# Optimization experiments

Measured on AMD Instinct MI355X. Metric: run time of the kernel, lower is better.

Reference implementation:

```python
import jax, jax.numpy as jnp
import numpy as np

N, T, U, D, V = 8, 200, 100, 512, 500


def setup_inputs() -> dict:
    key = jax.random.key(0)
    k1, k2, k3, k4 = jax.random.split(key, 4)
    encoder_out = jax.random.normal(k1, (N, T, D), dtype=jnp.float32)
    decoder_out = jax.random.normal(k2, (N, U, D), dtype=jnp.float32)
    # nn.Linear(input_dim, output_dim): weight (V, D), bias (V,)
    bound = 1.0 / np.sqrt(D)
    W = jax.random.uniform(k3, (V, D), minval=-bound, maxval=bound, dtype=jnp.float32)
    b = jax.random.uniform(k4, (V,), minval=-bound, maxval=bound, dtype=jnp.float32)
    return {"encoder_out": encoder_out, "decoder_out": decoder_out, "W": W, "b": b}


def reference(encoder_out, decoder_out, W, b):
    # broadcast add: (N,T,1,D) + (N,1,U,D) -> (N,T,U,D)
    x = encoder_out[:, :, None, :] + decoder_out[:, None, :, :]
    activations = jnp.tanh(x)
    # linear: (N,T,U,D) @ (D,V) + b -> (N,T,U,V)
    logits = jnp.einsum("ntud,vd->ntuv", activations, W) + b
    return logits
```

## Files before the change

### kernel.cpp

```cpp
#include <hip/hip_runtime.h>
#include <hip/hip_bf16.h>


#define NB 8
#define TT 200
#define UU 100
#define DD 512
#define VV 500
#define VP 512
#define BM 64
#define BK 32
#define KSTEPS 16
#define THREADS 256
#define LDA 40
#define MROWS (NB*TT*UU)
#define MBLOCKS (MROWS/BM)

typedef __attribute__((ext_vector_type(4))) float  f32x4;
typedef __attribute__((ext_vector_type(8))) short  s16x8;

__device__ __forceinline__ unsigned short f2bf(float f) {
    unsigned int u = __builtin_bit_cast(unsigned int, f);
    u = (u + 0x7FFFu + ((u >> 16) & 1u)) >> 16;
    return (unsigned short)u;
}

__device__ __forceinline__ float fast_tanh(float x) {
    float e = __expf(2.0f * x);
    return 1.0f - 2.0f * __builtin_amdgcn_rcpf(e + 1.0f);
}

__global__ void prep_w(const float* __restrict__ W, unsigned short* __restrict__ Wt) {
    int idx = blockIdx.x * 256 + threadIdx.x;
    int k = idx & 511;
    int v = idx >> 9;
    float val = (v < VV) ? W[v * DD + k] : 0.0f;
    Wt[(k >> 5) * (VP * BK) + v * BK + (k & 31)] = f2bf(val);
}

__global__ __launch_bounds__(THREADS, 2) void joiner_kernel(
    const float* __restrict__ enc, const float* __restrict__ dec,
    const unsigned short* __restrict__ Wt, const float* __restrict__ bias,
    float* __restrict__ out)
{
    __shared__ __align__(16) char smem[32000];
    unsigned short* lA0 = (unsigned short*)smem;
    unsigned short* lA1 = (unsigned short*)(smem + BM * LDA * 2);

    const int tid  = threadIdx.x;
    const int mb   = blockIdx.x;
    const int lane = tid & 63;
    const int wn   = tid >> 6;
    const int lr   = lane & 15;
    const int lk   = lane >> 4;

    const int srow = tid >> 2;
    const int sk   = (tid & 3) << 3;

    int r   = mb * BM + srow;
    int n   = r / (TT * UU);
    int rem = r - n * (TT * UU);
    int t   = rem / UU;
    int u   = rem - t * UU;
    const float* ep = enc + (n * TT + t) * DD + sk;
    const float* dp = dec + (n * UU + u) * DD + sk;

    f32x4 e0, e1, d0, d1;

    e0 = *(const f32x4*)(ep);     e1 = *(const f32x4*)(ep + 4);
    d0 = *(const f32x4*)(dp);     d1 = *(const f32x4*)(dp + 4);
    {
        s16x8 av;
        #pragma unroll
        for (int j = 0; j < 4; ++j) av[j]     = (short)f2bf(fast_tanh(e0[j] + d0[j]));
        #pragma unroll
        for (int j = 0; j < 4; ++j) av[4 + j] = (short)f2bf(fast_tanh(e1[j] + d1[j]));
        *(s16x8*)(&lA0[srow * LDA + sk]) = av;
    }
    e0 = *(const f32x4*)(ep + BK);     e1 = *(const f32x4*)(ep + BK + 4);
    d0 = *(const f32x4*)(dp + BK);     d1 = *(const f32x4*)(dp + BK + 4);
    __syncthreads();

    f32x4 acc[4][8];
    #pragma unroll
    for (int m = 0; m < 4; ++m)
        #pragma unroll
        for (int f = 0; f < 8; ++f)
            acc[m][f] = (f32x4){0.f, 0.f, 0.f, 0.f};

    const unsigned short* wptr = Wt + (wn * 128 + lr) * BK + lk * 8;

    for (int kc = 0; kc < KSTEPS; ++kc) {
        unsigned short* lCur = (kc & 1) ? lA1 : lA0;
        unsigned short* lNxt = (kc & 1) ? lA0 : lA1;

        s16x8 bF[8];
        #pragma unroll
        for (int f = 0; f < 8; ++f)
            bF[f] = *(const s16x8*)(wptr + kc * (VP * BK) + f * (16 * BK));

        s16x8 aF[4];
        #pragma unroll
        for (int m = 0; m < 4; ++m)
            aF[m] = *(const s16x8*)(&lCur[(m * 16 + lr) * LDA + lk * 8]);

        if (kc < KSTEPS - 1) {
            s16x8 av;
            #pragma unroll
            for (int j = 0; j < 4; ++j) av[j]     = (short)f2bf(fast_tanh(e0[j] + d0[j]));
            #pragma unroll
            for (int j = 0; j < 4; ++j) av[4 + j] = (short)f2bf(fast_tanh(e1[j] + d1[j]));
            *(s16x8*)(&lNxt[srow * LDA + sk]) = av;
            if (kc < KSTEPS - 2) {
                const float* ep2 = ep + (kc + 2) * BK;
                const float* dp2 = dp + (kc + 2) * BK;
                e0 = *(const f32x4*)(ep2);     e1 = *(const f32x4*)(ep2 + 4);
                d0 = *(const f32x4*)(dp2);     d1 = *(const f32x4*)(dp2 + 4);
            }
        }

        __builtin_amdgcn_s_setprio(1);
        #pragma unroll
        for (int m = 0; m < 4; ++m)
            #pragma unroll
            for (int f = 0; f < 8; ++f)
                acc[m][f] = __builtin_amdgcn_mfma_f32_16x16x32_bf16(aF[m], bF[f], acc[m][f], 0, 0, 0);
        __builtin_amdgcn_s_setprio(0);

        __syncthreads();
    }

    float bv[8];
    #pragma unroll
    for (int f = 0; f < 8; ++f) {
        int v = wn * 128 + f * 16 + lr;
        bv[f] = (v < VV) ? bias[v] : 0.0f;
    }

    float* lchunk = (float*)smem;
    float* outbase = out + (long)mb * BM * VV;

    for (int m = 0; m < 4; ++m) {
        __syncthreads();
        #pragma unroll
        for (int f = 0; f < 8; ++f) {
            int v = wn * 128 + f * 16 + lr;
            if (v < VV) {
                #pragma unroll
                for (int q = 0; q < 4; ++q)
                    lchunk[(lk * 4 + q) * VV + v] = acc[m][f][q] + bv[f];
            }
        }
        __syncthreads();
        float* dst = outbase + m * 16 * VV;
        #pragma unroll
        for (int i = 0; i < 8; ++i) {
            int c = i * THREADS + tid;
            if (c < 2000)
                *(f32x4*)(dst + c * 4) = *(const f32x4*)(lchunk + c * 4);
        }
    }
}

extern "C" void kernel_launch(void* const* d_in, const int* in_sizes, int n_in,
                              void* d_out, int out_size, void* d_ws, size_t ws_size,
                              hipStream_t stream) {
    const float* enc = (const float*)d_in[0];
    const float* dec = (const float*)d_in[1];
    const float* W   = (const float*)d_in[2];
    const float* b   = (const float*)d_in[3];
    float* out = (float*)d_out;
    unsigned short* Wt = (unsigned short*)d_ws;

    prep_w<<<dim3((VP * DD) / 256), dim3(256), 0, stream>>>(W, Wt);
    joiner_kernel<<<dim3(MBLOCKS), dim3(THREADS), 0, stream>>>(enc, dec, Wt, b, out);
}
```

Baseline: 144.6 us.

## Split vocab dimension across two blocks to halve accumulators and raise occupancy

Each block now covers 256 of the 500 vocab columns, using a 2D grid, instead of all of them. This halves the per-wave accumulator and B-fragment registers, and the launch bounds are raised to allow 3 blocks per SM. The staging buffer for the output is resized to a padded 264-float row. The cost is that every block recomputes the tanh activations for its rows and loads encoder and decoder data twice, so activation work and input traffic double.

```diff
diff --git a/kernel.cpp b/kernel.cpp
--- a/kernel.cpp
+++ b/kernel.cpp
@@ -9,10 +9,12 @@
 #define VV 500
 #define VP 512
 #define BM 64
+#define BNB 256
 #define BK 32
 #define KSTEPS 16
 #define THREADS 256
 #define LDA 40
+#define LCH 264
 #define MROWS (NB*TT*UU)
 #define MBLOCKS (MROWS/BM)
 
@@ -38,17 +40,18 @@
     Wt[(k >> 5) * (VP * BK) + v * BK + (k & 31)] = f2bf(val);
 }
 
-__global__ __launch_bounds__(THREADS, 2) void joiner_kernel(
+__global__ __launch_bounds__(THREADS, 3) void joiner_kernel(
     const float* __restrict__ enc, const float* __restrict__ dec,
     const unsigned short* __restrict__ Wt, const float* __restrict__ bias,
     float* __restrict__ out)
 {
-    __shared__ __align__(16) char smem[32000];
+    __shared__ __align__(16) char smem[16 * LCH * 4];
     unsigned short* lA0 = (unsigned short*)smem;
     unsigned short* lA1 = (unsigned short*)(smem + BM * LDA * 2);
 
     const int tid  = threadIdx.x;
     const int mb   = blockIdx.x;
+    const int vb   = blockIdx.y;
     const int lane = tid & 63;
     const int wn   = tid >> 6;
     const int lr   = lane & 15;
@@ -81,22 +84,22 @@
     d0 = *(const f32x4*)(dp + BK);     d1 = *(const f32x4*)(dp + BK + 4);
     __syncthreads();
 
-    f32x4 acc[4][8];
+    f32x4 acc[4][4];
     #pragma unroll
     for (int m = 0; m < 4; ++m)
         #pragma unroll
-        for (int f = 0; f < 8; ++f)
+        for (int f = 0; f < 4; ++f)
             acc[m][f] = (f32x4){0.f, 0.f, 0.f, 0.f};
 
-    const unsigned short* wptr = Wt + (wn * 128 + lr) * BK + lk * 8;
+    const unsigned short* wptr = Wt + (vb * BNB + wn * 64 + lr) * BK + lk * 8;
 
     for (int kc = 0; kc < KSTEPS; ++kc) {
         unsigned short* lCur = (kc & 1) ? lA1 : lA0;
         unsigned short* lNxt = (kc & 1) ? lA0 : lA1;
 
-        s16x8 bF[8];
+        s16x8 bF[4];
         #pragma unroll
-        for (int f = 0; f < 8; ++f)
+        for (int f = 0; f < 4; ++f)
             bF[f] = *(const s16x8*)(wptr + kc * (VP * BK) + f * (16 * BK));
 
         s16x8 aF[4];
@@ -123,41 +126,44 @@
         #pragma unroll
         for (int m = 0; m < 4; ++m)
             #pragma unroll
-            for (int f = 0; f < 8; ++f)
+            for (int f = 0; f < 4; ++f)
                 acc[m][f] = __builtin_amdgcn_mfma_f32_16x16x32_bf16(aF[m], bF[f], acc[m][f], 0, 0, 0);
         __builtin_amdgcn_s_setprio(0);
 
         __syncthreads();
     }
 
-    float bv[8];
+    float bv[4];
     #pragma unroll
-    for (int f = 0; f < 8; ++f) {
-        int v = wn * 128 + f * 16 + lr;
+    for (int f = 0; f < 4; ++f) {
+        int v = vb * BNB + wn * 64 + f * 16 + lr;
         bv[f] = (v < VV) ? bias[v] : 0.0f;
     }
 
     float* lchunk = (float*)smem;
-    float* outbase = out + (long)mb * BM * VV;
+    const int slabcols = (vb == 0) ? BNB : (VV - BNB);
+    const int segmax   = slabcols >> 2;
+    float* outbase = out + (long)mb * BM * VV + vb * BNB;
 
-    for (int m = 0; m < 4; ++m) {
+    for (int c = 0; c < 4; ++c) {
         __syncthreads();
         #pragma unroll
-        for (int f = 0; f < 8; ++f) {
-            int v = wn * 128 + f * 16 + lr;
-            if (v < VV) {
-                #pragma unroll
-                for (int q = 0; q < 4; ++q)
-                    lchunk[(lk * 4 + q) * VV + v] = acc[m][f][q] + bv[f];
-            }
+        for (int f = 0; f < 4; ++f) {
+            int vloc = wn * 64 + f * 16 + lr;
+            #pragma unroll
+            for (int q = 0; q < 4; ++q)
+                lchunk[(lk * 4 + q) * LCH + vloc] = acc[c][f][q] + bv[f];
         }
         __syncthreads();
-        float* dst = outbase + m * 16 * VV;
+        float* dst = outbase + c * 16 * VV;
         #pragma unroll
-        for (int i = 0; i < 8; ++i) {
-            int c = i * THREADS + tid;
-            if (c < 2000)
-                *(f32x4*)(dst + c * 4) = *(const f32x4*)(lchunk + c * 4);
+        for (int i = 0; i < 4; ++i) {
+            int idx = i * THREADS + tid;
+            int row = idx >> 6;
+            int seg = idx & 63;
+            if (seg < segmax)
+                *(f32x4*)(dst + row * VV + seg * 4) =
+                    *(const f32x4*)(lchunk + row * LCH + seg * 4);
         }
     }
 }
@@ -173,5 +179,5 @@
     unsigned short* Wt = (unsigned short*)d_ws;
 
     prep_w<<<dim3((VP * DD) / 256), dim3(256), 0, stream>>>(W, Wt);
-    joiner_kernel<<<dim3(MBLOCKS), dim3(THREADS), 0, stream>>>(enc, dec, Wt, b, out);
+    joiner_kernel<<<dim3(MBLOCKS, 2), dim3(THREADS), 0, stream>>>(enc, dec, Wt, b, out);
 }
```

Result: slower. 157.3 us (+8.8%).

## Split tanh activation into separate pass and tile GEMM over vocab halves

Applied to the files above, without the earlier changes.

When the workspace is large enough, the code first materialises the bf16 tanh activations for all 160k rows to global memory. A separate GEMM kernel then reads A fragments directly from global memory and splits the vocab dimension across two blocks, using 128x256 tiles with 512 threads. This removes per-block redundant tanh work and LDS staging of A, but adds roughly 160 MB of extra global writes and reads. The old fused kernel stays as the fallback when the workspace is too small.

```diff
diff --git a/kernel.cpp b/kernel.cpp
--- a/kernel.cpp
+++ b/kernel.cpp
@@ -8,13 +8,7 @@
 #define DD 512
 #define VV 500
 #define VP 512
-#define BM 64
-#define BK 32
-#define KSTEPS 16
-#define THREADS 256
-#define LDA 40
 #define MROWS (NB*TT*UU)
-#define MBLOCKS (MROWS/BM)
 
 typedef __attribute__((ext_vector_type(4))) float  f32x4;
 typedef __attribute__((ext_vector_type(8))) short  s16x8;
@@ -35,17 +29,133 @@
     int k = idx & 511;
     int v = idx >> 9;
     float val = (v < VV) ? W[v * DD + k] : 0.0f;
-    Wt[(k >> 5) * (VP * BK) + v * BK + (k & 31)] = f2bf(val);
-}
-
-__global__ __launch_bounds__(THREADS, 2) void joiner_kernel(
+    Wt[(k >> 5) * (VP * 32) + v * 32 + (k & 31)] = f2bf(val);
+}
+
+
+#define T1GRID 4096
+__global__ __launch_bounds__(256) void tanh_act(
+    const float* __restrict__ enc, const float* __restrict__ dec,
+    unsigned short* __restrict__ act)
+{
+    const int total = MROWS * (DD / 8);
+    for (int idx = blockIdx.x * 256 + threadIdx.x; idx < total;
+         idx += T1GRID * 256) {
+        int row = idx >> 6;
+        int k8  = (idx & 63) << 3;
+        int n   = row / (TT * UU);
+        int rem = row - n * (TT * UU);
+        int t   = rem / UU;
+        int u   = rem - t * UU;
+        const float* ep = enc + (n * TT + t) * DD + k8;
+        const float* dp = dec + (n * UU + u) * DD + k8;
+        f32x4 e0 = *(const f32x4*)(ep);
+        f32x4 e1 = *(const f32x4*)(ep + 4);
+        f32x4 d0 = *(const f32x4*)(dp);
+        f32x4 d1 = *(const f32x4*)(dp + 4);
+        s16x8 av;
+        #pragma unroll
+        for (int j = 0; j < 4; ++j) av[j]     = (short)f2bf(fast_tanh(e0[j] + d0[j]));
+        #pragma unroll
+        for (int j = 0; j < 4; ++j) av[4 + j] = (short)f2bf(fast_tanh(e1[j] + d1[j]));
+        *(s16x8*)(act + (long)row * DD + k8) = av;
+    }
+}
+
+#define GLCH 264
+__global__ __launch_bounds__(512, 4) void gemm_split(
+    const unsigned short* __restrict__ act, const unsigned short* __restrict__ Wt,
+    const float* __restrict__ bias, float* __restrict__ out)
+{
+    __shared__ __align__(16) float lchunk[32 * GLCH];
+
+    const int tid  = threadIdx.x;
+    const int mb   = blockIdx.x;
+    const int vb   = blockIdx.y;
+    const int lane = tid & 63;
+    const int w    = tid >> 6;
+    const int wm   = w >> 2;
+    const int wn   = w & 3;
+    const int lr   = lane & 15;
+    const int lk   = lane >> 4;
+
+    f32x4 acc[4][4];
+    #pragma unroll
+    for (int m = 0; m < 4; ++m)
+        #pragma unroll
+        for (int f = 0; f < 4; ++f)
+            acc[m][f] = (f32x4){0.f, 0.f, 0.f, 0.f};
+
+    const unsigned short* aptr = act + (long)(mb * 128 + wm * 64 + lr) * DD + lk * 8;
+    const unsigned short* wptr = Wt + (vb * 256 + wn * 64 + lr) * 32 + lk * 8;
+
+    for (int kc = 0; kc < 16; ++kc) {
+        s16x8 aF[4], bF[4];
+        #pragma unroll
+        for (int f = 0; f < 4; ++f)
+            bF[f] = *(const s16x8*)(wptr + kc * (VP * 32) + f * (16 * 32));
+        #pragma unroll
+        for (int m = 0; m < 4; ++m)
+            aF[m] = *(const s16x8*)(aptr + (long)(m * 16) * DD + kc * 32);
+
+        __builtin_amdgcn_s_setprio(1);
+        #pragma unroll
+        for (int m = 0; m < 4; ++m)
+            #pragma unroll
+            for (int f = 0; f < 4; ++f)
+                acc[m][f] = __builtin_amdgcn_mfma_f32_16x16x32_bf16(aF[m], bF[f], acc[m][f], 0, 0, 0);
+        __builtin_amdgcn_s_setprio(0);
+    }
+
+    float bv[4];
+    #pragma unroll
+    for (int f = 0; f < 4; ++f) {
+        int v = vb * 256 + wn * 64 + f * 16 + lr;
+        bv[f] = (v < VV) ? bias[v] : 0.0f;
+    }
+    const int slabcols = (vb == 0) ? 256 : (VV - 256);
+    const int segmax   = slabcols >> 2;
+    float* outbase = out + (long)mb * 128 * VV + vb * 256;
+
+    for (int c = 0; c < 4; ++c) {
+        if (c) __syncthreads();
+        if (wm == (c >> 1)) {
+            #pragma unroll
+            for (int mm = 0; mm < 2; ++mm) {
+                int m = (c & 1) * 2 + mm;
+                #pragma unroll
+                for (int f = 0; f < 4; ++f) {
+                    int vloc = wn * 64 + f * 16 + lr;
+                    #pragma unroll
+                    for (int q = 0; q < 4; ++q)
+                        lchunk[(mm * 16 + lk * 4 + q) * GLCH + vloc] = acc[m][f][q] + bv[f];
+                }
+            }
+        }
+        __syncthreads();
+        float* dst = outbase + (long)c * 32 * VV;
+        #pragma unroll
+        for (int i = 0; i < 4; ++i) {
+            int idx2 = i * 512 + tid;
+            int rw = idx2 >> 6;
+            int sg = idx2 & 63;
+            if (sg < segmax)
+                *(f32x4*)(dst + (long)rw * VV + sg * 4) =
+                    *(const f32x4*)(lchunk + rw * GLCH + sg * 4);
+        }
+    }
+}
+
+#define FBM 64
+#define FLDA 40
+__global__ __launch_bounds__(256, 2) void joiner_fused(
     const float* __restrict__ enc, const float* __restrict__ dec,
     const unsigned short* __restrict__ Wt, const float* __restrict__ bias,
     float* __restrict__ out)
 {
     __shared__ __align__(16) char smem[32000];
     unsigned short* lA0 = (unsigned short*)smem;
-    unsigned short* lA1 = (unsigned short*)(smem + BM * LDA * 2);
+    unsigned short* lA1 = (unsigned short*)(smem + FBM * FLDA * 2);
 
     const int tid  = threadIdx.x;
     const int mb   = blockIdx.x;
@@ -53,11 +163,10 @@
     const int wn   = tid >> 6;
     const int lr   = lane & 15;
     const int lk   = lane >> 4;
-
     const int srow = tid >> 2;
     const int sk   = (tid & 3) << 3;
 
-    int r   = mb * BM + srow;
+    int r   = mb * FBM + srow;
     int n   = r / (TT * UU);
     int rem = r - n * (TT * UU);
     int t   = rem / UU;
@@ -66,7 +175,6 @@
     const float* dp = dec + (n * UU + u) * DD + sk;
 
     f32x4 e0, e1, d0, d1;
-
     e0 = *(const f32x4*)(ep);     e1 = *(const f32x4*)(ep + 4);
     d0 = *(const f32x4*)(dp);     d1 = *(const f32x4*)(dp + 4);
     {
@@ -75,10 +183,10 @@
         for (int j = 0; j < 4; ++j) av[j]     = (short)f2bf(fast_tanh(e0[j] + d0[j]));
         #pragma unroll
         for (int j = 0; j < 4; ++j) av[4 + j] = (short)f2bf(fast_tanh(e1[j] + d1[j]));
-        *(s16x8*)(&lA0[srow * LDA + sk]) = av;
-    }
-    e0 = *(const f32x4*)(ep + BK);     e1 = *(const f32x4*)(ep + BK + 4);
-    d0 = *(const f32x4*)(dp + BK);     d1 = *(const f32x4*)(dp + BK + 4);
+        *(s16x8*)(&lA0[srow * FLDA + sk]) = av;
+    }
+    e0 = *(const f32x4*)(ep + 32);     e1 = *(const f32x4*)(ep + 36);
+    d0 = *(const f32x4*)(dp + 32);     d1 = *(const f32x4*)(dp + 36);
     __syncthreads();
 
     f32x4 acc[4][8];
@@ -88,32 +196,32 @@
         for (int f = 0; f < 8; ++f)
             acc[m][f] = (f32x4){0.f, 0.f, 0.f, 0.f};
 
-    const unsigned short* wptr = Wt + (wn * 128 + lr) * BK + lk * 8;
-
-    for (int kc = 0; kc < KSTEPS; ++kc) {
+    const unsigned short* wptr = Wt + (wn * 128 + lr) * 32 + lk * 8;
+
+    for (int kc = 0; kc < 16; ++kc) {
         unsigned short* lCur = (kc & 1) ? lA1 : lA0;
         unsigned short* lNxt = (kc & 1) ? lA0 : lA1;
 
         s16x8 bF[8];
         #pragma unroll
         for (int f = 0; f < 8; ++f)
-            bF[f] = *(const s16x8*)(wptr + kc * (VP * BK) + f * (16 * BK));
+            bF[f] = *(const s16x8*)(wptr + kc * (VP * 32) + f * (16 * 32));
 
         s16x8 aF[4];
         #pragma unroll
         for (int m = 0; m < 4; ++m)
-            aF[m] = *(const s16x8*)(&lCur[(m * 16 + lr) * LDA + lk * 8]);
-
-        if (kc < KSTEPS - 1) {
+            aF[m] = *(const s16x8*)(&lCur[(m * 16 + lr) * FLDA + lk * 8]);
+
+        if (kc < 15) {
             s16x8 av;
             #pragma unroll
             for (int j = 0; j < 4; ++j) av[j]     = (short)f2bf(fast_tanh(e0[j] + d0[j]));
             #pragma unroll
             for (int j = 0; j < 4; ++j) av[4 + j] = (short)f2bf(fast_tanh(e1[j] + d1[j]));
-            *(s16x8*)(&lNxt[srow * LDA + sk]) = av;
-            if (kc < KSTEPS - 2) {
-                const float* ep2 = ep + (kc + 2) * BK;
-                const float* dp2 = dp + (kc + 2) * BK;
+            *(s16x8*)(&lNxt[srow * FLDA + sk]) = av;
+            if (kc < 14) {
+                const float* ep2 = ep + (kc + 2) * 32;
+                const float* dp2 = dp + (kc + 2) * 32;
                 e0 = *(const f32x4*)(ep2);     e1 = *(const f32x4*)(ep2 + 4);
                 d0 = *(const f32x4*)(dp2);     d1 = *(const f32x4*)(dp2 + 4);
             }
@@ -138,7 +246,7 @@
     }
 
     float* lchunk = (float*)smem;
-    float* outbase = out + (long)mb * BM * VV;
+    float* outbase = out + (long)mb * FBM * VV;
 
     for (int m = 0; m < 4; ++m) {
         __syncthreads();
@@ -155,7 +263,7 @@
         float* dst = outbase + m * 16 * VV;
         #pragma unroll
         for (int i = 0; i < 8; ++i) {
-            int c = i * THREADS + tid;
+            int c = i * 256 + tid;
             if (c < 2000)
                 *(f32x4*)(dst + c * 4) = *(const f32x4*)(lchunk + c * 4);
         }
@@ -170,8 +278,19 @@
     const float* W   = (const float*)d_in[2];
     const float* b   = (const float*)d_in[3];
     float* out = (float*)d_out;
-    unsigned short* Wt = (unsigned short*)d_ws;
-
-    prep_w<<<dim3((VP * DD) / 256), dim3(256), 0, stream>>>(W, Wt);
-    joiner_kernel<<<dim3(MBLOCKS), dim3(THREADS), 0, stream>>>(enc, dec, Wt, b, out);
-}
+
+    const size_t actBytes = (size_t)MROWS * DD * 2;
+    const size_t wtBytes  = (size_t)VP * DD * 2;
+
+    if (ws_size >= actBytes + wtBytes) {
+        unsigned short* act = (unsigned short*)d_ws;
+        unsigned short* Wt  = (unsigned short*)((char*)d_ws + actBytes);
+        prep_w<<<dim3((VP * DD) / 256), dim3(256), 0, stream>>>(W, Wt);
+        tanh_act<<<dim3(T1GRID), dim3(256), 0, stream>>>(enc, dec, act);
+        gemm_split<<<dim3(MROWS / 128, 2), dim3(512), 0, stream>>>(act, Wt, b, out);
+    } else {
+        unsigned short* Wt = (unsigned short*)d_ws;
+        prep_w<<<dim3((VP * DD) / 256), dim3(256), 0, stream>>>(W, Wt);
+        joiner_fused<<<dim3(MROWS / FBM), dim3(256), 0, stream>>>(enc, dec, Wt, b, out);
+    }
+}
```

Result: slower. 350.7 us (+142.6%).

## Compute tanh activations directly into MFMA A-fragments, drop LDS staging

Applied to the files above, without the earlier changes.

Each wave now loads encoder/decoder values for its own A-fragment rows, applies tanh and packs to bf16 with v_cvt_pk_bf16_f32 directly in registers. This removes the LDS double buffer and the per-k-step __syncthreads. The tanh is also rewritten with exp2 and an fma. In exchange, each of the 4 waves recomputes the same 64xK tanh tile, so transcendental work is four times higher. Global loads also lose the one-step-ahead prefetch and now sit on the critical path before the MFMAs.

```diff
diff --git a/kernel.cpp b/kernel.cpp
--- a/kernel.cpp
+++ b/kernel.cpp
@@ -12,12 +12,12 @@
 #define BK 32
 #define KSTEPS 16
 #define THREADS 256
-#define LDA 40
 #define MROWS (NB*TT*UU)
 #define MBLOCKS (MROWS/BM)
 
-typedef __attribute__((ext_vector_type(4))) float  f32x4;
-typedef __attribute__((ext_vector_type(8))) short  s16x8;
+typedef __attribute__((ext_vector_type(4))) float         f32x4;
+typedef __attribute__((ext_vector_type(8))) short         s16x8;
+typedef __attribute__((ext_vector_type(4))) unsigned int  u32x4;
 
 __device__ __forceinline__ unsigned short f2bf(float f) {
     unsigned int u = __builtin_bit_cast(unsigned int, f);
@@ -25,9 +25,15 @@
     return (unsigned short)u;
 }
 
+__device__ __forceinline__ unsigned int cvt_pk_bf16(float a, float b) {
+    unsigned int r;
+    asm("v_cvt_pk_bf16_f32 %0, %1, %2" : "=v"(r) : "v"(a), "v"(b));
+    return r;
+}
+
 __device__ __forceinline__ float fast_tanh(float x) {
-    float e = __expf(2.0f * x);
-    return 1.0f - 2.0f * __builtin_amdgcn_rcpf(e + 1.0f);
+    float e = __builtin_amdgcn_exp2f(x * 2.88539008177793f);
+    return __builtin_fmaf(-2.0f, __builtin_amdgcn_rcpf(e + 1.0f), 1.0f);
 }
 
 __global__ void prep_w(const float* __restrict__ W, unsigned short* __restrict__ Wt) {
@@ -43,9 +49,7 @@
     const unsigned short* __restrict__ Wt, const float* __restrict__ bias,
     float* __restrict__ out)
 {
-    __shared__ __align__(16) char smem[32000];
-    unsigned short* lA0 = (unsigned short*)smem;
-    unsigned short* lA1 = (unsigned short*)(smem + BM * LDA * 2);
+    __shared__ __align__(16) float lchunk[16 * VV];
 
     const int tid  = threadIdx.x;
     const int mb   = blockIdx.x;
@@ -54,32 +58,18 @@
     const int lr   = lane & 15;
     const int lk   = lane >> 4;
 
-    const int srow = tid >> 2;
-    const int sk   = (tid & 3) << 3;
-
-    int r   = mb * BM + srow;
-    int n   = r / (TT * UU);
-    int rem = r - n * (TT * UU);
-    int t   = rem / UU;
-    int u   = rem - t * UU;
-    const float* ep = enc + (n * TT + t) * DD + sk;
-    const float* dp = dec + (n * UU + u) * DD + sk;
-
-    f32x4 e0, e1, d0, d1;
-
-    e0 = *(const f32x4*)(ep);     e1 = *(const f32x4*)(ep + 4);
-    d0 = *(const f32x4*)(dp);     d1 = *(const f32x4*)(dp + 4);
-    {
-        s16x8 av;
-        #pragma unroll
-        for (int j = 0; j < 4; ++j) av[j]     = (short)f2bf(fast_tanh(e0[j] + d0[j]));
-        #pragma unroll
-        for (int j = 0; j < 4; ++j) av[4 + j] = (short)f2bf(fast_tanh(e1[j] + d1[j]));
-        *(s16x8*)(&lA0[srow * LDA + sk]) = av;
+    const float* ep[4];
+    const float* dp[4];
+    #pragma unroll
+    for (int m = 0; m < 4; ++m) {
+        int r   = mb * BM + m * 16 + lr;
+        int n   = r / (TT * UU);
+        int rem = r - n * (TT * UU);
+        int t   = rem / UU;
+        int u   = rem - t * UU;
+        ep[m] = enc + (n * TT + t) * DD + lk * 8;
+        dp[m] = dec + (n * UU + u) * DD + lk * 8;
     }
-    e0 = *(const f32x4*)(ep + BK);     e1 = *(const f32x4*)(ep + BK + 4);
-    d0 = *(const f32x4*)(dp + BK);     d1 = *(const f32x4*)(dp + BK + 4);
-    __syncthreads();
 
     f32x4 acc[4][8];
     #pragma unroll
@@ -91,9 +81,6 @@
     const unsigned short* wptr = Wt + (wn * 128 + lr) * BK + lk * 8;
 
     for (int kc = 0; kc < KSTEPS; ++kc) {
-        unsigned short* lCur = (kc & 1) ? lA1 : lA0;
-        unsigned short* lNxt = (kc & 1) ? lA0 : lA1;
-
         s16x8 bF[8];
         #pragma unroll
         for (int f = 0; f < 8; ++f)
@@ -101,22 +88,27 @@
 
         s16x8 aF[4];
         #pragma unroll
-        for (int m = 0; m < 4; ++m)
-            aF[m] = *(const s16x8*)(&lCur[(m * 16 + lr) * LDA + lk * 8]);
-
-        if (kc < KSTEPS - 1) {
-            s16x8 av;
-            #pragma unroll
-            for (int j = 0; j < 4; ++j) av[j]     = (short)f2bf(fast_tanh(e0[j] + d0[j]));
-            #pragma unroll
-            for (int j = 0; j < 4; ++j) av[4 + j] = (short)f2bf(fast_tanh(e1[j] + d1[j]));
-            *(s16x8*)(&lNxt[srow * LDA + sk]) = av;
-            if (kc < KSTEPS - 2) {
-                const float* ep2 = ep + (kc + 2) * BK;
-                const float* dp2 = dp + (kc + 2) * BK;
-                e0 = *(const f32x4*)(ep2);     e1 = *(const f32x4*)(ep2 + 4);
-                d0 = *(const f32x4*)(dp2);     d1 = *(const f32x4*)(dp2 + 4);
-            }
+        for (int m = 0; m < 4; ++m) {
+            const float* e = ep[m] + kc * BK;
+            const float* d = dp[m] + kc * BK;
+            f32x4 e0 = *(const f32x4*)(e);
+            f32x4 e1 = *(const f32x4*)(e + 4);
+            f32x4 d0 = *(const f32x4*)(d);
+            f32x4 d1 = *(const f32x4*)(d + 4);
+            float t0 = fast_tanh(e0[0] + d0[0]);
+            float t1 = fast_tanh(e0[1] + d0[1]);
+            float t2 = fast_tanh(e0[2] + d0[2]);
+            float t3 = fast_tanh(e0[3] + d0[3]);
+            float t4 = fast_tanh(e1[0] + d1[0]);
+            float t5 = fast_tanh(e1[1] + d1[1]);
+            float t6 = fast_tanh(e1[2] + d1[2]);
+            float t7 = fast_tanh(e1[3] + d1[3]);
+            u32x4 wds;
+            wds[0] = cvt_pk_bf16(t0, t1);
+            wds[1] = cvt_pk_bf16(t2, t3);
+            wds[2] = cvt_pk_bf16(t4, t5);
+            wds[3] = cvt_pk_bf16(t6, t7);
+            aF[m] = __builtin_bit_cast(s16x8, wds);
         }
 
         __builtin_amdgcn_s_setprio(1);
@@ -126,8 +118,6 @@
             for (int f = 0; f < 8; ++f)
                 acc[m][f] = __builtin_amdgcn_mfma_f32_16x16x32_bf16(aF[m], bF[f], acc[m][f], 0, 0, 0);
         __builtin_amdgcn_s_setprio(0);
-
-        __syncthreads();
     }
 
     float bv[8];
@@ -137,7 +127,6 @@
         bv[f] = (v < VV) ? bias[v] : 0.0f;
     }
 
-    float* lchunk = (float*)smem;
     float* outbase = out + (long)mb * BM * VV;
 
     for (int m = 0; m < 4; ++m) {
```

After: 278.0 us. 1.92x slower.
